# Kernel tuning notes

Hardware: AMD Instinct MI355X
Metric: run time of the kernel (lower is better)

## Reference

```python
import jax, jax.numpy as jnp
import numpy as np

D = 1024      # neural_dim
M = 8192      # memory_size (assumed fully used)
H = 16        # num_heads
B = 64        # batch
HD = D // H   # head dim


def setup_inputs() -> dict:
    key = jax.random.key(0)
    ks = jax.random.split(key, 24)
    s = 0.02
    inp = {
        "neural_input": jax.random.normal(ks[0], (B, D), jnp.float32),
        "memory_keys": jax.random.normal(ks[1], (M, D), jnp.float32),
        "memory_values": jax.random.normal(ks[2], (M, D), jnp.float32),
        # query/key/value projections (nn.Linear weights are [out, in])
        "Wq": jax.random.normal(ks[3], (D, D), jnp.float32) * s,
        "bq": jnp.zeros((D,), jnp.float32),
        "Wk": jax.random.normal(ks[4], (D, D), jnp.float32) * s,
        "bk": jnp.zeros((D,), jnp.float32),
        "Wv": jax.random.normal(ks[5], (D, D), jnp.float32) * s,
        "bv": jnp.zeros((D,), jnp.float32),
        # MultiheadAttention packed in-projection [3D, D] and out projection
        "in_proj_w": jax.random.normal(ks[6], (3 * D, D), jnp.float32) * s,
        "in_proj_b": jnp.zeros((3 * D,), jnp.float32),
        "out_w": jax.random.normal(ks[7], (D, D), jnp.float32) * s,
        "out_b": jnp.zeros((D,), jnp.float32),
        # memory_gate: Linear(2D->D), ReLU, Linear(D->D), Sigmoid
        "gW1": jax.random.normal(ks[8], (D, 2 * D), jnp.float32) * s,
        "gb1": jnp.zeros((D,), jnp.float32),
        "gW2": jax.random.normal(ks[9], (D, D), jnp.float32) * s,
        "gb2": jnp.zeros((D,), jnp.float32),
        # integration: Linear(2D->2D), ReLU, Linear(2D->D)
        "iW1": jax.random.normal(ks[10], (2 * D, 2 * D), jnp.float32) * s,
        "ib1": jnp.zeros((2 * D,), jnp.float32),
        "iW2": jax.random.normal(ks[11], (D, 2 * D), jnp.float32) * s,
        "ib2": jnp.zeros((D,), jnp.float32),
    }
    return inp


def reference(neural_input, memory_keys, memory_values,
              Wq, bq, Wk, bk, Wv, bv,
              in_proj_w, in_proj_b, out_w, out_b,
              gW1, gb1, gW2, gb2, iW1, ib1, iW2, ib2):
    x = neural_input  # [B, D]
    # pre-projections (memory_used assumed all True -> full tables)
    q = x @ Wq.T + bq                  # [B, D]
    k = memory_keys @ Wk.T + bk        # [M, D]
    v = memory_values @ Wv.T + bv      # [M, D]

    # MultiheadAttention (single query per batch element; K/V shared
    # across batch instead of the redundant expand in the original)
    Wiq, Wik, Wiv = in_proj_w[:D], in_proj_w[D:2 * D], in_proj_w[2 * D:]
    biq, bik, biv = in_proj_b[:D], in_proj_b[D:2 * D], in_proj_b[2 * D:]
    qh = (q @ Wiq.T + biq).reshape(B, H, HD)   # [B, H, hd]
    kh = (k @ Wik.T + bik).reshape(M, H, HD)   # [M, H, hd]
    vh = (v @ Wiv.T + biv).reshape(M, H, HD)   # [M, H, hd]

    scale = 1.0 / np.sqrt(HD).astype(np.float32)
    scores = jnp.einsum('bhd,mhd->bhm', qh, kh) * scale  # [B, H, M]
    attn = jax.nn.softmax(scores, axis=-1)
    ctx = jnp.einsum('bhm,mhd->bhd', attn, vh).reshape(B, D)
    memory_signal = ctx @ out_w.T + out_b      # [B, D]

    # gated fusion
    gate_in = jnp.concatenate([x, memory_signal], axis=-1)          # [B, 2D]
    gate = jax.nn.sigmoid(jax.nn.relu(gate_in @ gW1.T + gb1) @ gW2.T + gb2)
    gated_memory = gate * memory_signal
    combined = jnp.concatenate([x, gated_memory], axis=-1)          # [B, 2D]
    out = jax.nn.relu(combined @ iW1.T + ib1) @ iW2.T + ib2         # [B, D]
    return out
```

## Files before the change

### kernel.cpp

```cpp
#include <hip/hip_runtime.h>
#include <hip/hip_bf16.h>
#include <stdint.h>


typedef __bf16 bf16;
typedef __bf16 bf16x4 __attribute__((ext_vector_type(4)));
typedef __bf16 bf16x8 __attribute__((ext_vector_type(8)));
typedef float f32x4 __attribute__((ext_vector_type(4)));

#define D_ 1024
#define M_ 8192
#define B_ 64
#define H_ 16

static __device__ __forceinline__ void gload16(const void* g, void* l) {
  __builtin_amdgcn_global_load_lds(
      (const __attribute__((address_space(1))) void*)g,
      (__attribute__((address_space(3))) void*)l, 16, 0, 0);
}

static __device__ __forceinline__ f32x4 mfma16(bf16x8 a, bf16x8 b, f32x4 c) {
  return __builtin_amdgcn_mfma_f32_16x16x32_bf16(a, b, c, 0, 0, 0);
}

template <int U, int KLEN, typename OutT>
__device__ __forceinline__ void thin_gemm(
    const bf16* __restrict__ A, int lda,
    const bf16* __restrict__ Bm, int ldb,
    OutT* __restrict__ C, int ldc,
    const float* __restrict__ bias, float scale) {
  const int tid = threadIdx.x, lane = tid & 63, w = tid >> 6;
  const int rl = lane & 15, qq = lane >> 4;
  const bf16* pa = A + (int64_t)(w * 16 + rl) * lda + qq * 8;
  const bf16* pb[4];
  pb[0] = Bm + (int64_t)rl * ldb + qq * 8;
  pb[1] = pb[0] + (int64_t)16 * ldb;
  pb[2] = pb[0] + (int64_t)32 * ldb;
  pb[3] = pb[0] + (int64_t)48 * ldb;
  f32x4 acc[4] = {};
  bf16x8 av[2][U], bv[2][U][4];
#pragma unroll
  for (int u = 0; u < U; u++) {
    av[0][u] = *(const bf16x8*)(pa + u * 32);
#pragma unroll
    for (int j = 0; j < 4; j++)
      bv[0][u][j] = *(const bf16x8*)(pb[j] + u * 32);
  }
  constexpr int NI = KLEN / (32 * U);
#pragma unroll
  for (int it = 0; it < NI; it++) {
    const int cur = it & 1, nxt = cur ^ 1;
    if (it + 1 < NI) {
      int k = (it + 1) * 32 * U;
#pragma unroll
      for (int u = 0; u < U; u++) {
        av[nxt][u] = *(const bf16x8*)(pa + k + u * 32);
#pragma unroll
        for (int j = 0; j < 4; j++)
          bv[nxt][u][j] = *(const bf16x8*)(pb[j] + k + u * 32);
      }
    }
#pragma unroll
    for (int u = 0; u < U; u++)
#pragma unroll
      for (int j = 0; j < 4; j++)
        acc[j] = mfma16(av[cur][u], bv[cur][u][j], acc[j]);
  }
#pragma unroll
  for (int j = 0; j < 4; j++) {
    int gn = j * 16 + rl;
    float bb = bias ? bias[gn] : 0.0f;
#pragma unroll
    for (int r = 0; r < 4; r++) {
      int gm = w * 16 + qq * 4 + r;
      C[(int64_t)gm * ldc + gn] = (OutT)((acc[j][r] + bb) * scale);
    }
  }
}

struct CvtD { const float* src; bf16* dst; int end; };
struct PrepArgs {
  CvtD d[9];
  const float *Wq, *Wk, *Wv, *inw, *inb, *bq, *bk, *bv;
  bf16* WT;
  float* bc;
};

__global__ __launch_bounds__(256) void prep_kernel(PrepArgs a) {
  const int bx = blockIdx.x, tid = threadIdx.x;
  if (bx < 29760) {
    int g = bx * 256 + tid;
    CvtD dd = a.d[8];
    int begin = a.d[7].end;
#pragma unroll
    for (int t = 7; t >= 0; t--)
      if (g < a.d[t].end) { dd = a.d[t]; begin = t ? a.d[t - 1].end : 0; }
    int i = (g - begin) * 4;
    float4 v = *(const float4*)(dd.src + i);
    bf16x4 o = { (bf16)v.x, (bf16)v.y, (bf16)v.z, (bf16)v.w };
    *(bf16x4*)(dd.dst + i) = o;
  } else if (bx < 32832) {
    int t = bx - 29760;
    int z = t >> 10, rem = t & 1023;
    const float* src = z == 0 ? a.Wq : z == 1 ? a.Wk : a.Wv;
    bf16* out = a.WT + (int64_t)z * D_ * D_;
    __shared__ bf16 tile[32][33];
    int tx = tid & 31, ty = tid >> 5;
    int r0 = (rem >> 5) * 32, c0 = (rem & 31) * 32;
#pragma unroll
    for (int i = 0; i < 32; i += 8)
      tile[ty + i][tx] = (bf16)src[(int64_t)(r0 + ty + i) * D_ + c0 + tx];
    __syncthreads();
#pragma unroll
    for (int i = 0; i < 32; i += 8)
      out[(int64_t)(c0 + ty + i) * D_ + r0 + tx] = tile[tx][ty + i];
  } else {
    int t = bx - 32832;
    int w = tid >> 6, lane = tid & 63;
    int ng = t * 4 + w;
    int z = ng >> 10;
    const float* Wi = a.inw + (int64_t)ng * D_;
    const float* b = z == 0 ? a.bq : z == 1 ? a.bk : a.bv;
    float acc = 0.f;
#pragma unroll
    for (int l = 0; l < D_; l += 64) acc += Wi[l + lane] * b[l + lane];
#pragma unroll
    for (int m = 32; m; m >>= 1) acc += __shfl_xor(acc, m, 64);
    if (lane == 0) a.bc[ng] = acc + a.inb[ng];
  }
}

__global__ __launch_bounds__(256) void init_bias(
    const float* __restrict__ outb, const float* __restrict__ gb1,
    const float* __restrict__ gb2, const float* __restrict__ ib1,
    const float* __restrict__ ib2, float* __restrict__ msR,
    float* __restrict__ g1R, float* __restrict__ gateR,
    float* __restrict__ h1R, float* __restrict__ out) {
  int c = (blockIdx.x * 256 + threadIdx.x) * 4;
  int row = blockIdx.y;
  const float* b; float* dst; int n;
  if (c < 1024)      { b = outb; dst = msR   + row * 1024; n = c; }
  else if (c < 2048) { b = gb1;  dst = g1R   + row * 1024; n = c - 1024; }
  else if (c < 3072) { b = gb2;  dst = gateR + row * 1024; n = c - 2048; }
  else if (c < 5120) { b = ib1;  dst = h1R   + row * 2048; n = c - 3072; }
  else               { b = ib2;  dst = out   + row * 1024; n = c - 5120; }
  *(float4*)(dst + n) = *(const float4*)(b + n);
}

template <int MODE>
__global__ __launch_bounds__(256) void gemm_big(
    const bf16* __restrict__ A, int lda, int64_t sA,
    const bf16* __restrict__ Bm, int ldb, int64_t sB,
    bf16* __restrict__ C, int ldc, bf16* __restrict__ Ct,
    const float* __restrict__ bias, int64_t sbias, int K,
    const bf16* __restrict__ qA, const bf16* __restrict__ qB,
    bf16* __restrict__ qC, const float* __restrict__ qbias) {
  int m0, n0, z;
  if (MODE == 0) {
    z = blockIdx.z; m0 = blockIdx.y * 128; n0 = blockIdx.x * 128;
  } else {
    if ((int)blockIdx.x >= 1024) {
      int n0q = ((int)blockIdx.x - 1024) * 64;
      thin_gemm<2, 1024, bf16>(qA, D_, qB + (int64_t)n0q * D_, D_,
                               qC + n0q, D_, qbias + n0q, 0.125f);
      return;
    }
    int lin = blockIdx.x, xcd = lin & 7, slot = lin >> 3;
    z = slot >> 6;
    int r = slot & 63;
    m0 = (xcd * 8 + (r >> 3)) * 128;
    n0 = (r & 7) * 128;
  }
  A += (int64_t)z * sA; Bm += (int64_t)z * sB;
  if (bias) bias += (int64_t)z * sbias;
  __shared__ alignas(16) bf16 As[128 * 64];
  __shared__ alignas(16) bf16 Bs[128 * 64];
  const int tid = threadIdx.x, lane = tid & 63, w = tid >> 6;
  const int wm = (w & 1) * 64, wn = (w >> 1) * 64;
  const int rl = lane & 15, qq = lane >> 4;
  f32x4 acc[4][4] = {};

  const bf16 *gA[4], *gB[4];
  bf16 *lA[4], *lB[4];
#pragma unroll
  for (int it = 0; it < 4; it++) {
    int cc = it * 256 + w * 64 + lane;
    int r = cc >> 3, qp = cc & 7, q = qp ^ (r & 7);
    gA[it] = A + (int64_t)(m0 + r) * lda + q * 8;
    gB[it] = Bm + (int64_t)(n0 + r) * ldb + q * 8;
    lA[it] = As + (it * 256 + w * 64) * 8;
    lB[it] = Bs + (it * 256 + w * 64) * 8;
  }
  for (int k0 = 0; k0 < K; k0 += 64) {
    __syncthreads();
#pragma unroll
    for (int it = 0; it < 4; it++) {
      gload16(gA[it] + k0, lA[it]);
      gload16(gB[it] + k0, lB[it]);
    }
    __syncthreads();
#pragma unroll
    for (int kk = 0; kk < 2; kk++) {
      bf16x8 af[4], bb[4];
#pragma unroll
      for (int i = 0; i < 4; i++) {
        int ar = wm + i * 16 + rl;
        af[i] = *(const bf16x8*)(As + ar * 64 + (((kk * 4 + qq) ^ (ar & 7)) * 8));
      }
#pragma unroll
      for (int j = 0; j < 4; j++) {
        int br = wn + j * 16 + rl;
        bb[j] = *(const bf16x8*)(Bs + br * 64 + (((kk * 4 + qq) ^ (br & 7)) * 8));
      }
#pragma unroll
      for (int i = 0; i < 4; i++)
#pragma unroll
        for (int j = 0; j < 4; j++)
          acc[i][j] = mfma16(af[i], bb[j], acc[i][j]);
    }
  }
  if (MODE == 1 && z == 1) {
#pragma unroll
    for (int j = 0; j < 4; j++) {
      int gn = n0 + wn + j * 16 + rl;
      float bb = bias ? bias[gn] : 0.0f;
#pragma unroll
      for (int i = 0; i < 4; i++) {
        int gm0 = m0 + wm + i * 16 + qq * 4;
        f32x4 a = acc[i][j];
        bf16x4 o = { (bf16)(a[0] + bb), (bf16)(a[1] + bb),
                     (bf16)(a[2] + bb), (bf16)(a[3] + bb) };
        *(bf16x4*)(Ct + (int64_t)gn * M_ + gm0) = o;
      }
    }
  } else {
#pragma unroll
    for (int j = 0; j < 4; j++) {
      int gn = n0 + wn + j * 16 + rl;
      float bb = bias ? bias[gn] : 0.0f;
#pragma unroll
      for (int i = 0; i < 4; i++) {
        int gm0 = m0 + wm + i * 16 + qq * 4;
#pragma unroll
        for (int r = 0; r < 4; r++)
          C[(int64_t)(gm0 + r) * ldc + gn] = (bf16)(acc[i][j][r] + bb);
      }
    }
  }
}

__global__ __launch_bounds__(256) void flash_kernel(
    const bf16* __restrict__ qh, const bf16* __restrict__ kh,
    const bf16* __restrict__ vhT, float* __restrict__ opart,
    float* __restrict__ ml) {
  const int tid = threadIdx.x, lane = tid & 63, w = tid >> 6;
  const int rl = lane & 15, qq = lane >> 4;
  const int h = blockIdx.x >> 4, c = blockIdx.x & 15;
  __shared__ alignas(16) bf16 Plds[4 * 16 * 72];
  const bf16* qhp = qh + (int64_t)(w * 16 + rl) * D_ + h * 64 + qq * 8;
  bf16x8 aq0 = *(const bf16x8*)(qhp);
  bf16x8 aq1 = *(const bf16x8*)(qhp + 32);
  float m_st[4], l_st[4];
  f32x4 acc_o[4] = {};
#pragma unroll
  for (int r = 0; r < 4; r++) { m_st[r] = -3.0e38f; l_st[r] = 0.f; }
  bf16* pl = Plds + w * 1152;
  const bf16* khb = kh + (int64_t)(c * 512) * D_ + h * 64 + qq * 8;
  const bf16* vtb = vhT + (int64_t)(h * 64) * M_ + c * 512 + qq * 8;
  for (int nt = 0; nt < 8; nt++) {
    int mb = nt * 64;
    bf16x8 bk0[4], bk1[4];
#pragma unroll
    for (int j = 0; j < 4; j++) {
      const bf16* p = khb + (int64_t)(mb + j * 16 + rl) * D_;
      bk0[j] = *(const bf16x8*)(p);
      bk1[j] = *(const bf16x8*)(p + 32);
    }
    f32x4 s[4] = {};
#pragma unroll
    for (int j = 0; j < 4; j++) {
      s[j] = mfma16(aq0, bk0[j], s[j]);
      s[j] = mfma16(aq1, bk1[j], s[j]);
    }
    float rmax[4], alpha[4], rsum[4];
#pragma unroll
    for (int r = 0; r < 4; r++)
      rmax[r] = fmaxf(fmaxf(s[0][r], s[1][r]), fmaxf(s[2][r], s[3][r]));
#pragma unroll
    for (int msk = 1; msk <= 8; msk <<= 1)
#pragma unroll
      for (int r = 0; r < 4; r++)
        rmax[r] = fmaxf(rmax[r], __shfl_xor(rmax[r], msk, 64));
#pragma unroll
    for (int r = 0; r < 4; r++) {
      float mn = fmaxf(m_st[r], rmax[r]);
      alpha[r] = __expf(m_st[r] - mn);
      m_st[r] = mn;
      rsum[r] = 0.f;
    }
#pragma unroll
    for (int j = 0; j < 4; j++)
#pragma unroll
      for (int r = 0; r < 4; r++) {
        float p = __expf(s[j][r] - m_st[r]);
        rsum[r] += p;
        pl[(qq * 4 + r) * 72 + j * 16 + rl] = (bf16)p;
      }
#pragma unroll
    for (int msk = 1; msk <= 8; msk <<= 1)
#pragma unroll
      for (int r = 0; r < 4; r++) rsum[r] += __shfl_xor(rsum[r], msk, 64);
#pragma unroll
    for (int r = 0; r < 4; r++) l_st[r] = l_st[r] * alpha[r] + rsum[r];
#pragma unroll
    for (int j = 0; j < 4; j++)
#pragma unroll
      for (int r = 0; r < 4; r++) acc_o[j][r] *= alpha[r];
    bf16x8 pa0 = *(const bf16x8*)(pl + rl * 72 + qq * 8);
    bf16x8 pa1 = *(const bf16x8*)(pl + rl * 72 + 32 + qq * 8);
#pragma unroll
    for (int j = 0; j < 4; j++) {
      const bf16* q = vtb + (int64_t)(j * 16 + rl) * M_ + mb;
      bf16x8 v0 = *(const bf16x8*)(q);
      bf16x8 v1 = *(const bf16x8*)(q + 32);
      acc_o[j] = mfma16(pa0, v0, acc_o[j]);
      acc_o[j] = mfma16(pa1, v1, acc_o[j]);
    }
  }
  float* op = opart + (int64_t)(h * 16 + c) * 64 * 64;
#pragma unroll
  for (int j = 0; j < 4; j++)
#pragma unroll
    for (int r = 0; r < 4; r++)
      op[(w * 16 + qq * 4 + r) * 64 + j * 16 + rl] = acc_o[j][r];
  if (rl == 0) {
    float* mlp = ml + (int64_t)(h * 16 + c) * 128;
#pragma unroll
    for (int r = 0; r < 4; r++) {
      mlp[w * 16 + qq * 4 + r] = m_st[r];
      mlp[64 + w * 16 + qq * 4 + r] = l_st[r];
    }
  }
}

__global__ __launch_bounds__(256) void combine_kernel(
    const float* __restrict__ opart, const float* __restrict__ ml,
    bf16* __restrict__ ctx) {
  const int h = blockIdx.x >> 2, g = blockIdx.x & 3;
  const int d = threadIdx.x & 63;
#pragma unroll
  for (int it = 0; it < 4; it++) {
    int b = g * 16 + (threadIdx.x >> 6) + it * 4;
    float mstar = -3.0e38f;
    float mv_[16], lv_[16];
#pragma unroll
    for (int cc = 0; cc < 16; cc++) {
      mv_[cc] = ml[(int64_t)(h * 16 + cc) * 128 + b];
      lv_[cc] = ml[(int64_t)(h * 16 + cc) * 128 + 64 + b];
      mstar = fmaxf(mstar, mv_[cc]);
    }
    float lsum = 0.f, osum = 0.f;
#pragma unroll
    for (int cc = 0; cc < 16; cc++) {
      float f = __expf(mv_[cc] - mstar);
      lsum += lv_[cc] * f;
      osum += opart[((int64_t)(h * 16 + cc) * 64 + b) * 64 + d] * f;
    }
    ctx[(int64_t)b * D_ + h * 64 + d] = (bf16)(osum / lsum);
  }
}

struct Chunk { const void* p0; const void* p1; int ld; int kind; };
struct StageArgs { Chunk c[8]; };

__global__ __launch_bounds__(256) void tail_stage(
    StageArgs sa, const bf16* __restrict__ Bw, int ldb,
    float* __restrict__ Craw, int ldc) {
  const int n0 = blockIdx.x * 64, kc = blockIdx.y;
  const Chunk ch = sa.c[kc];
  const int tid = threadIdx.x, lane = tid & 63, w = tid >> 6;
  const int rl = lane & 15, qq = lane >> 4;
  const int m = w * 16 + rl;
  const bf16* pb[4];
#pragma unroll
  for (int j = 0; j < 4; j++)
    pb[j] = Bw + (int64_t)(n0 + j * 16 + rl) * ldb + kc * 256 + qq * 8;
  f32x4 acc[4] = {};
#pragma unroll
  for (int kk = 0; kk < 8; kk++) {
    bf16x8 af;
    if (ch.kind == 0) {
      af = *(const bf16x8*)((const bf16*)ch.p0 + (int64_t)m * ch.ld +
                            kk * 32 + qq * 8);
    } else {
      const float* p = (const float*)ch.p0 + (int64_t)m * ch.ld + kk * 32 + qq * 8;
      float4 u0 = *(const float4*)p;
      float4 u1 = *(const float4*)(p + 4);
      if (ch.kind == 2) {
        u0.x = fmaxf(u0.x, 0.f); u0.y = fmaxf(u0.y, 0.f);
        u0.z = fmaxf(u0.z, 0.f); u0.w = fmaxf(u0.w, 0.f);
        u1.x = fmaxf(u1.x, 0.f); u1.y = fmaxf(u1.y, 0.f);
        u1.z = fmaxf(u1.z, 0.f); u1.w = fmaxf(u1.w, 0.f);
      } else if (ch.kind == 3) {
        const float* pm = (const float*)ch.p1 + (int64_t)m * ch.ld + kk * 32 + qq * 8;
        float4 m0 = *(const float4*)pm;
        float4 m1 = *(const float4*)(pm + 4);
        u0.x = m0.x / (1.f + __expf(-u0.x)); u0.y = m0.y / (1.f + __expf(-u0.y));
        u0.z = m0.z / (1.f + __expf(-u0.z)); u0.w = m0.w / (1.f + __expf(-u0.w));
        u1.x = m1.x / (1.f + __expf(-u1.x)); u1.y = m1.y / (1.f + __expf(-u1.y));
        u1.z = m1.z / (1.f + __expf(-u1.z)); u1.w = m1.w / (1.f + __expf(-u1.w));
      }
      af = (bf16x8){ (bf16)u0.x, (bf16)u0.y, (bf16)u0.z, (bf16)u0.w,
                     (bf16)u1.x, (bf16)u1.y, (bf16)u1.z, (bf16)u1.w };
    }
    bf16x8 bf_[4];
#pragma unroll
    for (int j = 0; j < 4; j++) bf_[j] = *(const bf16x8*)(pb[j] + kk * 32);
#pragma unroll
    for (int j = 0; j < 4; j++) acc[j] = mfma16(af, bf_[j], acc[j]);
  }
#pragma unroll
  for (int j = 0; j < 4; j++) {
    int gn = n0 + j * 16 + rl;
#pragma unroll
    for (int r = 0; r < 4; r++) {
      int gm = w * 16 + qq * 4 + r;
      atomicAdd(&Craw[(int64_t)gm * ldc + gn], acc[j][r]);
    }
  }
}

extern "C" void kernel_launch(void* const* d_in, const int* in_sizes, int n_in,
                              void* d_out, int out_size, void* d_ws,
                              size_t ws_size, hipStream_t stream) {
  (void)in_sizes; (void)n_in; (void)out_size;
  const float* x    = (const float*)d_in[0];
  const float* mk   = (const float*)d_in[1];
  const float* mv   = (const float*)d_in[2];
  const float* Wq   = (const float*)d_in[3];
  const float* bq   = (const float*)d_in[4];
  const float* Wk   = (const float*)d_in[5];
  const float* bk   = (const float*)d_in[6];
  const float* Wv   = (const float*)d_in[7];
  const float* bv   = (const float*)d_in[8];
  const float* inw  = (const float*)d_in[9];
  const float* inb  = (const float*)d_in[10];
  const float* outw = (const float*)d_in[11];
  const float* outb = (const float*)d_in[12];
  const float* gW1  = (const float*)d_in[13];
  const float* gb1  = (const float*)d_in[14];
  const float* gW2  = (const float*)d_in[15];
  const float* gb2  = (const float*)d_in[16];
  const float* iW1  = (const float*)d_in[17];
  const float* ib1  = (const float*)d_in[18];
  const float* iW2  = (const float*)d_in[19];
  const float* ib2  = (const float*)d_in[20];

  char* ws = (char*)d_ws;
  size_t off = 0;
  auto alloc = [&](size_t bytes) {
    char* p = ws + off;
    off += (bytes + 255) & ~(size_t)255;
    return p;
  };
  bf16* mkmv  = (bf16*)alloc((size_t)2 * M_ * D_ * 2);
  bf16* inpj  = (bf16*)alloc((size_t)3 * D_ * D_ * 2);
  bf16* WT    = (bf16*)alloc((size_t)3 * D_ * D_ * 2);
  bf16* Wc    = (bf16*)alloc((size_t)3 * D_ * D_ * 2);
  float* bc   = (float*)alloc(3 * D_ * 4);
  bf16* xbf   = (bf16*)alloc((size_t)B_ * D_ * 2);
  bf16* qh    = (bf16*)alloc((size_t)B_ * D_ * 2);
  bf16* kh    = (bf16*)alloc((size_t)M_ * D_ * 2);
  bf16* vhT   = (bf16*)alloc((size_t)M_ * D_ * 2);
  float* opart= (float*)alloc((size_t)H_ * 16 * 64 * 64 * 4);
  float* ml   = (float*)alloc((size_t)H_ * 16 * 128 * 4);
  bf16* ctx   = (bf16*)alloc((size_t)B_ * D_ * 2);
  float* msR  = (float*)alloc((size_t)B_ * D_ * 4);
  float* g1R  = (float*)alloc((size_t)B_ * D_ * 4);
  float* gateR= (float*)alloc((size_t)B_ * D_ * 4);
  float* h1R  = (float*)alloc((size_t)B_ * 2 * D_ * 4);
  bf16* gW1b  = (bf16*)alloc((size_t)D_ * 2 * D_ * 2);
  bf16* gW2b  = (bf16*)alloc((size_t)D_ * D_ * 2);
  bf16* iW1b  = (bf16*)alloc((size_t)2 * D_ * 2 * D_ * 2);
  bf16* iW2b  = (bf16*)alloc((size_t)D_ * 2 * D_ * 2);
  bf16* outwb = (bf16*)alloc((size_t)D_ * D_ * 2);
  if (ws_size < off) return;

  PrepArgs pa;
  pa.d[0] = { mk,   mkmv,           2097152 };
  pa.d[1] = { mv,   mkmv + M_ * D_, 4194304 };
  pa.d[2] = { inw,  inpj,           4980736 };
  pa.d[3] = { gW1,  gW1b,           5505024 };
  pa.d[4] = { gW2,  gW2b,           5767168 };
  pa.d[5] = { iW1,  iW1b,           6815744 };
  pa.d[6] = { iW2,  iW2b,           7340032 };
  pa.d[7] = { outw, outwb,          7602176 };
  pa.d[8] = { x,    xbf,            7618560 };
  pa.Wq = Wq; pa.Wk = Wk; pa.Wv = Wv; pa.inw = inw; pa.inb = inb;
  pa.bq = bq; pa.bk = bk; pa.bv = bv; pa.WT = WT; pa.bc = bc;
  prep_kernel<<<dim3(33600), 256, 0, stream>>>(pa);

  init_bias<<<dim3(6, 64), 256, 0, stream>>>(outb, gb1, gb2, ib1, ib2,
                                             msR, g1R, gateR, h1R,
                                             (float*)d_out);

  gemm_big<0><<<dim3(8, 8, 3), 256, 0, stream>>>(
      inpj, D_, (int64_t)D_ * D_, WT, D_, (int64_t)D_ * D_,
      Wc, D_, nullptr, nullptr, 0, D_, nullptr, nullptr, nullptr, nullptr);

  gemm_big<1><<<dim3(1040), 256, 0, stream>>>(
      mkmv, D_, (int64_t)M_ * D_, Wc + (int64_t)D_ * D_, D_, (int64_t)D_ * D_,
      kh, D_, vhT, bc + D_, D_, D_,
      xbf, Wc, qh, bc);

  flash_kernel<<<dim3(256), 256, 0, stream>>>(qh, kh, vhT, opart, ml);
  combine_kernel<<<dim3(64), 256, 0, stream>>>(opart, ml, ctx);

  StageArgs s7;
  for (int kc = 0; kc < 4; kc++) s7.c[kc] = { ctx + kc * 256, nullptr, D_, 0 };
  tail_stage<<<dim3(16, 4), 256, 0, stream>>>(s7, outwb, D_, msR, D_);

  StageArgs s8;
  for (int kc = 0; kc < 4; kc++) s8.c[kc] = { xbf + kc * 256, nullptr, D_, 0 };
  for (int kc = 4; kc < 8; kc++) s8.c[kc] = { msR + (kc - 4) * 256, nullptr, D_, 1 };
  tail_stage<<<dim3(16, 8), 256, 0, stream>>>(s8, gW1b, 2 * D_, g1R, D_);

  StageArgs s9;
  for (int kc = 0; kc < 4; kc++) s9.c[kc] = { g1R + kc * 256, nullptr, D_, 2 };
  tail_stage<<<dim3(16, 4), 256, 0, stream>>>(s9, gW2b, D_, gateR, D_);

  StageArgs s10;
  for (int kc = 0; kc < 4; kc++) s10.c[kc] = { xbf + kc * 256, nullptr, D_, 0 };
  for (int kc = 4; kc < 8; kc++)
    s10.c[kc] = { gateR + (kc - 4) * 256, msR + (kc - 4) * 256, D_, 3 };
  tail_stage<<<dim3(32, 8), 256, 0, stream>>>(s10, iW1b, 2 * D_, h1R, 2 * D_);

  StageArgs s11;
  for (int kc = 0; kc < 8; kc++) s11.c[kc] = { h1R + kc * 256, nullptr, 2 * D_, 2 };
  tail_stage<<<dim3(16, 8), 256, 0, stream>>>(s11, iW2b, 2 * D_,
                                              (float*)d_out, D_);
}
```

Before: 381.4 us.

## Fuse attention and MLP tail into persistent kernel with grid barriers, shrink GEMM K-tile

Merges the flash attention, combine and five tail GEMM stages into one persistent 256-block kernel that steps through the stages using an atomic-counter grid barrier. It also folds the bias-init kernel into the prep kernel and halves the big GEMM K-tile from 64 to 32 with a new LDS swizzle. The aim is to cut kernel-launch overhead and give the big GEMM a smaller LDS footprint. In exchange it relies on all 256 blocks being resident at once for the spin barrier, and the smaller K-tile doubles the number of sync steps.

```diff
diff --git a/kernel.cpp b/kernel.cpp
--- a/kernel.cpp
+++ b/kernel.cpp
@@ -82,12 +82,15 @@
 struct PrepArgs {
   CvtD d[9];
   const float *Wq, *Wk, *Wv, *inw, *inb, *bq, *bk, *bv;
+  const float *outb, *gb1, *gb2, *ib1, *ib2;
   bf16* WT;
-  float* bc;
+  float *bc, *msR, *g1R, *gateR, *h1R, *out;
+  unsigned* bar;
 };
 
 __global__ __launch_bounds__(256) void prep_kernel(PrepArgs a) {
   const int bx = blockIdx.x, tid = threadIdx.x;
+  if (bx == 0 && tid == 0) *a.bar = 0u;
   if (bx < 29760) {
     int g = bx * 256 + tid;
     CvtD dd = a.d[8];
@@ -114,7 +117,7 @@
 #pragma unroll
     for (int i = 0; i < 32; i += 8)
       out[(int64_t)(c0 + ty + i) * D_ + r0 + tx] = tile[tx][ty + i];
-  } else {
+  } else if (bx < 33600) {
     int t = bx - 32832;
     int w = tid >> 6, lane = tid & 63;
     int ng = t * 4 + w;
@@ -127,31 +130,28 @@
 #pragma unroll
     for (int m = 32; m; m >>= 1) acc += __shfl_xor(acc, m, 64);
     if (lane == 0) a.bc[ng] = acc + a.inb[ng];
-  }
-}
-
-__global__ __launch_bounds__(256) void init_bias(
-    const float* __restrict__ outb, const float* __restrict__ gb1,
-    const float* __restrict__ gb2, const float* __restrict__ ib1,
-    const float* __restrict__ ib2, float* __restrict__ msR,
-    float* __restrict__ g1R, float* __restrict__ gateR,
-    float* __restrict__ h1R, float* __restrict__ out) {
-  int c = (blockIdx.x * 256 + threadIdx.x) * 4;
-  int row = blockIdx.y;
-  const float* b; float* dst; int n;
-  if (c < 1024)      { b = outb; dst = msR   + row * 1024; n = c; }
-  else if (c < 2048) { b = gb1;  dst = g1R   + row * 1024; n = c - 1024; }
-  else if (c < 3072) { b = gb2;  dst = gateR + row * 1024; n = c - 2048; }
-  else if (c < 5120) { b = ib1;  dst = h1R   + row * 2048; n = c - 3072; }
-  else               { b = ib2;  dst = out   + row * 1024; n = c - 5120; }
-  *(float4*)(dst + n) = *(const float4*)(b + n);
+  } else {
+    int t = bx - 33600;
+    int seg = t >> 6, row = t & 63;
+    int n = tid * 4;
+    const float* b;
+    float* dst;
+    int bn = n;
+    if (seg == 0)      { dst = a.msR   + row * 1024;        b = a.outb; }
+    else if (seg == 1) { dst = a.g1R   + row * 1024;        b = a.gb1;  }
+    else if (seg == 2) { dst = a.gateR + row * 1024;        b = a.gb2;  }
+    else if (seg == 3) { dst = a.h1R   + row * 2048;        b = a.ib1;  }
+    else if (seg == 4) { dst = a.h1R   + row * 2048 + 1024; b = a.ib1; bn = 1024 + n; }
+    else               { dst = a.out   + row * 1024;        b = a.ib2;  }
+    *(float4*)(dst + n) = *(const float4*)(b + bn);
+  }
 }
 
 template <int MODE>
 __global__ __launch_bounds__(256) void gemm_big(
     const bf16* __restrict__ A, int lda, int64_t sA,
     const bf16* __restrict__ Bm, int ldb, int64_t sB,
-    bf16* __restrict__ C, int ldc, bf16* __restrict__ Ct,
+    bf16* __restrict__ C, int ldc, int64_t sC, bf16* __restrict__ Ct,
     const float* __restrict__ bias, int64_t sbias, int K,
     const bf16* __restrict__ qA, const bf16* __restrict__ qB,
     bf16* __restrict__ qC, const float* __restrict__ qbias) {
@@ -173,236 +173,110 @@
   }
   A += (int64_t)z * sA; Bm += (int64_t)z * sB;
   if (bias) bias += (int64_t)z * sbias;
-  __shared__ alignas(16) bf16 As[128 * 64];
-  __shared__ alignas(16) bf16 Bs[128 * 64];
+  __shared__ alignas(16) bf16 As[128 * 32];
+  __shared__ alignas(16) bf16 Bs[128 * 32];
   const int tid = threadIdx.x, lane = tid & 63, w = tid >> 6;
   const int wm = (w & 1) * 64, wn = (w >> 1) * 64;
   const int rl = lane & 15, qq = lane >> 4;
   f32x4 acc[4][4] = {};
 
-  const bf16 *gA[4], *gB[4];
-  bf16 *lA[4], *lB[4];
-#pragma unroll
-  for (int it = 0; it < 4; it++) {
-    int cc = it * 256 + w * 64 + lane;
-    int r = cc >> 3, qp = cc & 7, q = qp ^ (r & 7);
-    gA[it] = A + (int64_t)(m0 + r) * lda + q * 8;
-    gB[it] = Bm + (int64_t)(n0 + r) * ldb + q * 8;
-    lA[it] = As + (it * 256 + w * 64) * 8;
-    lB[it] = Bs + (it * 256 + w * 64) * 8;
-  }
-  for (int k0 = 0; k0 < K; k0 += 64) {
+  int c0 = w * 64 + lane, c1 = (4 + w) * 64 + lane;
+  int ra0 = c0 >> 2, qa0 = (c0 & 3) ^ ((ra0 >> 1) & 3);
+  int ra1 = c1 >> 2, qa1 = (c1 & 3) ^ ((ra1 >> 1) & 3);
+  const bf16* gA0 = A + (int64_t)(m0 + ra0) * lda + qa0 * 8;
+  const bf16* gA1 = A + (int64_t)(m0 + ra1) * lda + qa1 * 8;
+  const bf16* gB0 = Bm + (int64_t)(n0 + ra0) * ldb + qa0 * 8;
+  const bf16* gB1 = Bm + (int64_t)(n0 + ra1) * ldb + qa1 * 8;
+  bf16* lA0 = As + w * 512;
+  bf16* lA1 = As + (4 + w) * 512;
+  bf16* lB0 = Bs + w * 512;
+  bf16* lB1 = Bs + (4 + w) * 512;
+
+  for (int k0 = 0; k0 < K; k0 += 32) {
     __syncthreads();
-#pragma unroll
-    for (int it = 0; it < 4; it++) {
-      gload16(gA[it] + k0, lA[it]);
-      gload16(gB[it] + k0, lB[it]);
-    }
+    gload16(gA0 + k0, lA0);
+    gload16(gA1 + k0, lA1);
+    gload16(gB0 + k0, lB0);
+    gload16(gB1 + k0, lB1);
     __syncthreads();
-#pragma unroll
-    for (int kk = 0; kk < 2; kk++) {
-      bf16x8 af[4], bb[4];
-#pragma unroll
-      for (int i = 0; i < 4; i++) {
-        int ar = wm + i * 16 + rl;
-        af[i] = *(const bf16x8*)(As + ar * 64 + (((kk * 4 + qq) ^ (ar & 7)) * 8));
-      }
-#pragma unroll
-      for (int j = 0; j < 4; j++) {
-        int br = wn + j * 16 + rl;
-        bb[j] = *(const bf16x8*)(Bs + br * 64 + (((kk * 4 + qq) ^ (br & 7)) * 8));
-      }
-#pragma unroll
-      for (int i = 0; i < 4; i++)
-#pragma unroll
-        for (int j = 0; j < 4; j++)
-          acc[i][j] = mfma16(af[i], bb[j], acc[i][j]);
-    }
+    bf16x8 af[4], bb[4];
+#pragma unroll
+    for (int i = 0; i < 4; i++) {
+      int r = wm + i * 16 + rl;
+      af[i] = *(const bf16x8*)(As + r * 32 + (qq ^ ((r >> 1) & 3)) * 8);
+    }
+#pragma unroll
+    for (int j = 0; j < 4; j++) {
+      int r = wn + j * 16 + rl;
+      bb[j] = *(const bf16x8*)(Bs + r * 32 + (qq ^ ((r >> 1) & 3)) * 8);
+    }
+#pragma unroll
+    for (int i = 0; i < 4; i++)
+#pragma unroll
+      for (int j = 0; j < 4; j++)
+        acc[i][j] = mfma16(af[i], bb[j], acc[i][j]);
   }
   if (MODE == 1 && z == 1) {
 #pragma unroll
     for (int j = 0; j < 4; j++) {
       int gn = n0 + wn + j * 16 + rl;
-      float bb = bias ? bias[gn] : 0.0f;
+      float bb2 = bias ? bias[gn] : 0.0f;
 #pragma unroll
       for (int i = 0; i < 4; i++) {
         int gm0 = m0 + wm + i * 16 + qq * 4;
         f32x4 a = acc[i][j];
-        bf16x4 o = { (bf16)(a[0] + bb), (bf16)(a[1] + bb),
-                     (bf16)(a[2] + bb), (bf16)(a[3] + bb) };
+        bf16x4 o = { (bf16)(a[0] + bb2), (bf16)(a[1] + bb2),
+                     (bf16)(a[2] + bb2), (bf16)(a[3] + bb2) };
         *(bf16x4*)(Ct + (int64_t)gn * M_ + gm0) = o;
       }
     }
   } else {
+    C += (int64_t)z * sC;
 #pragma unroll
     for (int j = 0; j < 4; j++) {
       int gn = n0 + wn + j * 16 + rl;
-      float bb = bias ? bias[gn] : 0.0f;
+      float bb2 = bias ? bias[gn] : 0.0f;
 #pragma unroll
       for (int i = 0; i < 4; i++) {
         int gm0 = m0 + wm + i * 16 + qq * 4;
 #pragma unroll
         for (int r = 0; r < 4; r++)
-          C[(int64_t)(gm0 + r) * ldc + gn] = (bf16)(acc[i][j][r] + bb);
-      }
-    }
-  }
-}
-
-__global__ __launch_bounds__(256) void flash_kernel(
-    const bf16* __restrict__ qh, const bf16* __restrict__ kh,
-    const bf16* __restrict__ vhT, float* __restrict__ opart,
-    float* __restrict__ ml) {
-  const int tid = threadIdx.x, lane = tid & 63, w = tid >> 6;
-  const int rl = lane & 15, qq = lane >> 4;
-  const int h = blockIdx.x >> 4, c = blockIdx.x & 15;
-  __shared__ alignas(16) bf16 Plds[4 * 16 * 72];
-  const bf16* qhp = qh + (int64_t)(w * 16 + rl) * D_ + h * 64 + qq * 8;
-  bf16x8 aq0 = *(const bf16x8*)(qhp);
-  bf16x8 aq1 = *(const bf16x8*)(qhp + 32);
-  float m_st[4], l_st[4];
-  f32x4 acc_o[4] = {};
-#pragma unroll
-  for (int r = 0; r < 4; r++) { m_st[r] = -3.0e38f; l_st[r] = 0.f; }
-  bf16* pl = Plds + w * 1152;
-  const bf16* khb = kh + (int64_t)(c * 512) * D_ + h * 64 + qq * 8;
-  const bf16* vtb = vhT + (int64_t)(h * 64) * M_ + c * 512 + qq * 8;
-  for (int nt = 0; nt < 8; nt++) {
-    int mb = nt * 64;
-    bf16x8 bk0[4], bk1[4];
-#pragma unroll
-    for (int j = 0; j < 4; j++) {
-      const bf16* p = khb + (int64_t)(mb + j * 16 + rl) * D_;
-      bk0[j] = *(const bf16x8*)(p);
-      bk1[j] = *(const bf16x8*)(p + 32);
-    }
-    f32x4 s[4] = {};
-#pragma unroll
-    for (int j = 0; j < 4; j++) {
-      s[j] = mfma16(aq0, bk0[j], s[j]);
-      s[j] = mfma16(aq1, bk1[j], s[j]);
-    }
-    float rmax[4], alpha[4], rsum[4];
-#pragma unroll
-    for (int r = 0; r < 4; r++)
-      rmax[r] = fmaxf(fmaxf(s[0][r], s[1][r]), fmaxf(s[2][r], s[3][r]));
-#pragma unroll
-    for (int msk = 1; msk <= 8; msk <<= 1)
-#pragma unroll
-      for (int r = 0; r < 4; r++)
-        rmax[r] = fmaxf(rmax[r], __shfl_xor(rmax[r], msk, 64));
-#pragma unroll
-    for (int r = 0; r < 4; r++) {
-      float mn = fmaxf(m_st[r], rmax[r]);
-      alpha[r] = __expf(m_st[r] - mn);
-      m_st[r] = mn;
-      rsum[r] = 0.f;
-    }
-#pragma unroll
-    for (int j = 0; j < 4; j++)
-#pragma unroll
-      for (int r = 0; r < 4; r++) {
-        float p = __expf(s[j][r] - m_st[r]);
-        rsum[r] += p;
-        pl[(qq * 4 + r) * 72 + j * 16 + rl] = (bf16)p;
-      }
-#pragma unroll
-    for (int msk = 1; msk <= 8; msk <<= 1)
-#pragma unroll
-      for (int r = 0; r < 4; r++) rsum[r] += __shfl_xor(rsum[r], msk, 64);
-#pragma unroll
-    for (int r = 0; r < 4; r++) l_st[r] = l_st[r] * alpha[r] + rsum[r];
-#pragma unroll
-    for (int j = 0; j < 4; j++)
-#pragma unroll
-      for (int r = 0; r < 4; r++) acc_o[j][r] *= alpha[r];
-    bf16x8 pa0 = *(const bf16x8*)(pl + rl * 72 + qq * 8);
-    bf16x8 pa1 = *(const bf16x8*)(pl + rl * 72 + 32 + qq * 8);
-#pragma unroll
-    for (int j = 0; j < 4; j++) {
-      const bf16* q = vtb + (int64_t)(j * 16 + rl) * M_ + mb;
-      bf16x8 v0 = *(const bf16x8*)(q);
-      bf16x8 v1 = *(const bf16x8*)(q + 32);
-      acc_o[j] = mfma16(pa0, v0, acc_o[j]);
-      acc_o[j] = mfma16(pa1, v1, acc_o[j]);
-    }
-  }
-  float* op = opart + (int64_t)(h * 16 + c) * 64 * 64;
-#pragma unroll
-  for (int j = 0; j < 4; j++)
-#pragma unroll
-    for (int r = 0; r < 4; r++)
-      op[(w * 16 + qq * 4 + r) * 64 + j * 16 + rl] = acc_o[j][r];
-  if (rl == 0) {
-    float* mlp = ml + (int64_t)(h * 16 + c) * 128;
-#pragma unroll
-    for (int r = 0; r < 4; r++) {
-      mlp[w * 16 + qq * 4 + r] = m_st[r];
-      mlp[64 + w * 16 + qq * 4 + r] = l_st[r];
-    }
-  }
-}
-
-__global__ __launch_bounds__(256) void combine_kernel(
-    const float* __restrict__ opart, const float* __restrict__ ml,
-    bf16* __restrict__ ctx) {
-  const int h = blockIdx.x >> 2, g = blockIdx.x & 3;
-  const int d = threadIdx.x & 63;
-#pragma unroll
-  for (int it = 0; it < 4; it++) {
-    int b = g * 16 + (threadIdx.x >> 6) + it * 4;
-    float mstar = -3.0e38f;
-    float mv_[16], lv_[16];
-#pragma unroll
-    for (int cc = 0; cc < 16; cc++) {
-      mv_[cc] = ml[(int64_t)(h * 16 + cc) * 128 + b];
-      lv_[cc] = ml[(int64_t)(h * 16 + cc) * 128 + 64 + b];
-      mstar = fmaxf(mstar, mv_[cc]);
-    }
-    float lsum = 0.f, osum = 0.f;
-#pragma unroll
-    for (int cc = 0; cc < 16; cc++) {
-      float f = __expf(mv_[cc] - mstar);
-      lsum += lv_[cc] * f;
-      osum += opart[((int64_t)(h * 16 + cc) * 64 + b) * 64 + d] * f;
-    }
-    ctx[(int64_t)b * D_ + h * 64 + d] = (bf16)(osum / lsum);
-  }
-}
-
-struct Chunk { const void* p0; const void* p1; int ld; int kind; };
-struct StageArgs { Chunk c[8]; };
-
-__global__ __launch_bounds__(256) void tail_stage(
-    StageArgs sa, const bf16* __restrict__ Bw, int ldb,
+          C[(int64_t)(gm0 + r) * ldc + gn] = (bf16)(acc[i][j][r] + bb2);
+      }
+    }
+  }
+}
+
+template <int KIND, int NKK>
+static __device__ __forceinline__ void stage_mm(
+    const void* __restrict__ p0, const void* __restrict__ p1, int lda,
+    const bf16* __restrict__ Bw, int ldb, int bk0, int n0,
     float* __restrict__ Craw, int ldc) {
-  const int n0 = blockIdx.x * 64, kc = blockIdx.y;
-  const Chunk ch = sa.c[kc];
   const int tid = threadIdx.x, lane = tid & 63, w = tid >> 6;
   const int rl = lane & 15, qq = lane >> 4;
   const int m = w * 16 + rl;
   const bf16* pb[4];
 #pragma unroll
   for (int j = 0; j < 4; j++)
-    pb[j] = Bw + (int64_t)(n0 + j * 16 + rl) * ldb + kc * 256 + qq * 8;
+    pb[j] = Bw + (int64_t)(n0 + j * 16 + rl) * ldb + bk0 + qq * 8;
   f32x4 acc[4] = {};
 #pragma unroll
-  for (int kk = 0; kk < 8; kk++) {
+  for (int kk = 0; kk < NKK; kk++) {
     bf16x8 af;
-    if (ch.kind == 0) {
-      af = *(const bf16x8*)((const bf16*)ch.p0 + (int64_t)m * ch.ld +
-                            kk * 32 + qq * 8);
+    if constexpr (KIND == 0) {
+      af = *(const bf16x8*)((const bf16*)p0 + (int64_t)m * lda + kk * 32 + qq * 8);
     } else {
-      const float* p = (const float*)ch.p0 + (int64_t)m * ch.ld + kk * 32 + qq * 8;
+      const float* p = (const float*)p0 + (int64_t)m * lda + kk * 32 + qq * 8;
       float4 u0 = *(const float4*)p;
       float4 u1 = *(const float4*)(p + 4);
-      if (ch.kind == 2) {
+      if constexpr (KIND == 2) {
         u0.x = fmaxf(u0.x, 0.f); u0.y = fmaxf(u0.y, 0.f);
         u0.z = fmaxf(u0.z, 0.f); u0.w = fmaxf(u0.w, 0.f);
         u1.x = fmaxf(u1.x, 0.f); u1.y = fmaxf(u1.y, 0.f);
         u1.z = fmaxf(u1.z, 0.f); u1.w = fmaxf(u1.w, 0.f);
-      } else if (ch.kind == 3) {
-        const float* pm = (const float*)ch.p1 + (int64_t)m * ch.ld + kk * 32 + qq * 8;
+      }
+      if constexpr (KIND == 3) {
+        const float* pm = (const float*)p1 + (int64_t)m * lda + kk * 32 + qq * 8;
         float4 m0 = *(const float4*)pm;
         float4 m1 = *(const float4*)(pm + 4);
         u0.x = m0.x / (1.f + __expf(-u0.x)); u0.y = m0.y / (1.f + __expf(-u0.y));
@@ -427,6 +301,192 @@
       int gm = w * 16 + qq * 4 + r;
       atomicAdd(&Craw[(int64_t)gm * ldc + gn], acc[j][r]);
     }
+  }
+}
+
+struct TailArgs {
+  const bf16 *qh, *kh, *vhT, *xbf;
+  float *opart, *ml;
+  bf16* ctx;
+  const bf16 *outwb, *gW1b, *gW2b, *iW1b, *iW2b;
+  float *msR, *g1R, *gateR, *h1R, *out;
+  unsigned* bar;
+};
+
+static __device__ __forceinline__ void grid_sync(unsigned* bar, unsigned target) {
+  __syncthreads();
+  if (threadIdx.x == 0) {
+    __threadfence();
+    atomicAdd(bar, 1u);
+    while (__hip_atomic_load(bar, __ATOMIC_RELAXED, __HIP_MEMORY_SCOPE_AGENT) <
+           target)
+      __builtin_amdgcn_s_sleep(2);
+    __threadfence();
+  }
+  __syncthreads();
+}
+
+__global__ __launch_bounds__(256, 1) void tail_mega(TailArgs ta) {
+  const int bx = blockIdx.x;
+  const int tid = threadIdx.x, lane = tid & 63, w = tid >> 6;
+  const int rl = lane & 15, qq = lane >> 4;
+  __shared__ alignas(16) bf16 Plds[4 * 16 * 72];
+
+  {
+    const int h = bx >> 4, c = bx & 15;
+    const bf16* qhp = ta.qh + (int64_t)(w * 16 + rl) * D_ + h * 64 + qq * 8;
+    bf16x8 aq0 = *(const bf16x8*)(qhp);
+    bf16x8 aq1 = *(const bf16x8*)(qhp + 32);
+    float m_st[4], l_st[4];
+    f32x4 acc_o[4] = {};
+#pragma unroll
+    for (int r = 0; r < 4; r++) { m_st[r] = -3.0e38f; l_st[r] = 0.f; }
+    bf16* pl = Plds + w * 1152;
+    const bf16* khb = ta.kh + (int64_t)(c * 512) * D_ + h * 64 + qq * 8;
+    const bf16* vtb = ta.vhT + (int64_t)(h * 64) * M_ + c * 512 + qq * 8;
+    for (int nt = 0; nt < 8; nt++) {
+      int mb = nt * 64;
+      bf16x8 bk0[4], bk1[4];
+#pragma unroll
+      for (int j = 0; j < 4; j++) {
+        const bf16* p = khb + (int64_t)(mb + j * 16 + rl) * D_;
+        bk0[j] = *(const bf16x8*)(p);
+        bk1[j] = *(const bf16x8*)(p + 32);
+      }
+      f32x4 s[4] = {};
+#pragma unroll
+      for (int j = 0; j < 4; j++) {
+        s[j] = mfma16(aq0, bk0[j], s[j]);
+        s[j] = mfma16(aq1, bk1[j], s[j]);
+      }
+      float rmax[4], alpha[4], rsum[4];
+#pragma unroll
+      for (int r = 0; r < 4; r++)
+        rmax[r] = fmaxf(fmaxf(s[0][r], s[1][r]), fmaxf(s[2][r], s[3][r]));
+#pragma unroll
+      for (int msk = 1; msk <= 8; msk <<= 1)
+#pragma unroll
+        for (int r = 0; r < 4; r++)
+          rmax[r] = fmaxf(rmax[r], __shfl_xor(rmax[r], msk, 64));
+#pragma unroll
+      for (int r = 0; r < 4; r++) {
+        float mn = fmaxf(m_st[r], rmax[r]);
+        alpha[r] = __expf(m_st[r] - mn);
+        m_st[r] = mn;
+        rsum[r] = 0.f;
+      }
+#pragma unroll
+      for (int j = 0; j < 4; j++)
+#pragma unroll
+        for (int r = 0; r < 4; r++) {
+          float p = __expf(s[j][r] - m_st[r]);
+          rsum[r] += p;
+          pl[(qq * 4 + r) * 72 + j * 16 + rl] = (bf16)p;
+        }
+#pragma unroll
+      for (int msk = 1; msk <= 8; msk <<= 1)
+#pragma unroll
+        for (int r = 0; r < 4; r++) rsum[r] += __shfl_xor(rsum[r], msk, 64);
+#pragma unroll
+      for (int r = 0; r < 4; r++) l_st[r] = l_st[r] * alpha[r] + rsum[r];
+#pragma unroll
+      for (int j = 0; j < 4; j++)
+#pragma unroll
+        for (int r = 0; r < 4; r++) acc_o[j][r] *= alpha[r];
+      bf16x8 pa0 = *(const bf16x8*)(pl + rl * 72 + qq * 8);
+      bf16x8 pa1 = *(const bf16x8*)(pl + rl * 72 + 32 + qq * 8);
+#pragma unroll
+      for (int j = 0; j < 4; j++) {
+        const bf16* q = vtb + (int64_t)(j * 16 + rl) * M_ + mb;
+        bf16x8 v0 = *(const bf16x8*)(q);
+        bf16x8 v1 = *(const bf16x8*)(q + 32);
+        acc_o[j] = mfma16(pa0, v0, acc_o[j]);
+        acc_o[j] = mfma16(pa1, v1, acc_o[j]);
+      }
+    }
+    float* op = ta.opart + (int64_t)(h * 16 + c) * 64 * 64;
+#pragma unroll
+    for (int j = 0; j < 4; j++)
+#pragma unroll
+      for (int r = 0; r < 4; r++)
+        op[(w * 16 + qq * 4 + r) * 64 + j * 16 + rl] = acc_o[j][r];
+    if (rl == 0) {
+      float* mlp = ta.ml + (int64_t)(h * 16 + c) * 128;
+#pragma unroll
+      for (int r = 0; r < 4; r++) {
+        mlp[w * 16 + qq * 4 + r] = m_st[r];
+        mlp[64 + w * 16 + qq * 4 + r] = l_st[r];
+      }
+    }
+  }
+  grid_sync(ta.bar, 256);
+
+  if (bx < 64) {
+    const int h = bx >> 2, g = bx & 3;
+    const int d = tid & 63;
+#pragma unroll
+    for (int it = 0; it < 4; it++) {
+      int b = g * 16 + (tid >> 6) + it * 4;
+      float mstar = -3.0e38f;
+      float mv_[16], lv_[16];
+#pragma unroll
+      for (int cc = 0; cc < 16; cc++) {
+        mv_[cc] = ta.ml[(int64_t)(h * 16 + cc) * 128 + b];
+        lv_[cc] = ta.ml[(int64_t)(h * 16 + cc) * 128 + 64 + b];
+        mstar = fmaxf(mstar, mv_[cc]);
+      }
+      float lsum = 0.f, osum = 0.f;
+#pragma unroll
+      for (int cc = 0; cc < 16; cc++) {
+        float f = __expf(mv_[cc] - mstar);
+        lsum += lv_[cc] * f;
+        osum += ta.opart[((int64_t)(h * 16 + cc) * 64 + b) * 64 + d] * f;
+      }
+      ta.ctx[(int64_t)b * D_ + h * 64 + d] = (bf16)(osum / lsum);
+    }
+  }
+  grid_sync(ta.bar, 512);
+
+  {
+    int n0 = (bx >> 4) * 64, kc = bx & 15;
+    stage_mm<0, 2>(ta.ctx + kc * 64, nullptr, D_, ta.outwb, D_, kc * 64, n0,
+                   ta.msR, D_);
+  }
+  grid_sync(ta.bar, 768);
+
+  {
+    int n0 = (bx >> 4) * 64, kc = bx & 15;
+    if (kc < 8)
+      stage_mm<0, 4>(ta.xbf + kc * 128, nullptr, D_, ta.gW1b, 2048, kc * 128,
+                     n0, ta.g1R, D_);
+    else
+      stage_mm<1, 4>(ta.msR + (kc - 8) * 128, nullptr, D_, ta.gW1b, 2048,
+                     1024 + (kc - 8) * 128, n0, ta.g1R, D_);
+  }
+  grid_sync(ta.bar, 1024);
+
+  {
+    int n0 = (bx >> 4) * 64, kc = bx & 15;
+    stage_mm<2, 2>(ta.g1R + kc * 64, nullptr, D_, ta.gW2b, D_, kc * 64, n0,
+                   ta.gateR, D_);
+  }
+  grid_sync(ta.bar, 1280);
+
+  {
+    int n0 = (bx >> 3) * 64, kc = bx & 7;
+    if (kc < 4)
+      stage_mm<0, 8>(ta.xbf + kc * 256, nullptr, D_, ta.iW1b, 2048, kc * 256,
+                     n0, ta.h1R, 2048);
+    else
+      stage_mm<3, 8>(ta.gateR + (kc - 4) * 256, ta.msR + (kc - 4) * 256, D_,
+                     ta.iW1b, 2048, 1024 + (kc - 4) * 256, n0, ta.h1R, 2048);
+  }
+  grid_sync(ta.bar, 1536);
+
+  {
+    int n0 = (bx >> 4) * 64, kc = bx & 15;
+    stage_mm<2, 4>(ta.h1R + kc * 128, nullptr, 2048, ta.iW2b, 2048, kc * 128,
+                   n0, ta.out, D_);
   }
 }
 
@@ -484,6 +544,7 @@
   bf16* iW1b  = (bf16*)alloc((size_t)2 * D_ * 2 * D_ * 2);
   bf16* iW2b  = (bf16*)alloc((size_t)D_ * 2 * D_ * 2);
   bf16* outwb = (bf16*)alloc((size_t)D_ * D_ * 2);
+  unsigned* bar = (unsigned*)alloc(256);
   if (ws_size < off) return;
 
   PrepArgs pa;
@@ -497,46 +558,28 @@
   pa.d[7] = { outw, outwb,          7602176 };
   pa.d[8] = { x,    xbf,            7618560 };
   pa.Wq = Wq; pa.Wk = Wk; pa.Wv = Wv; pa.inw = inw; pa.inb = inb;
-  pa.bq = bq; pa.bk = bk; pa.bv = bv; pa.WT = WT; pa.bc = bc;
-  prep_kernel<<<dim3(33600), 256, 0, stream>>>(pa);
-
-  init_bias<<<dim3(6, 64), 256, 0, stream>>>(outb, gb1, gb2, ib1, ib2,
-                                             msR, g1R, gateR, h1R,
-                                             (float*)d_out);
+  pa.bq = bq; pa.bk = bk; pa.bv = bv;
+  pa.outb = outb; pa.gb1 = gb1; pa.gb2 = gb2; pa.ib1 = ib1; pa.ib2 = ib2;
+  pa.WT = WT; pa.bc = bc; pa.msR = msR; pa.g1R = g1R; pa.gateR = gateR;
+  pa.h1R = h1R; pa.out = (float*)d_out; pa.bar = bar;
+  prep_kernel<<<dim3(33984), 256, 0, stream>>>(pa);
 
   gemm_big<0><<<dim3(8, 8, 3), 256, 0, stream>>>(
       inpj, D_, (int64_t)D_ * D_, WT, D_, (int64_t)D_ * D_,
-      Wc, D_, nullptr, nullptr, 0, D_, nullptr, nullptr, nullptr, nullptr);
+      Wc, D_, (int64_t)D_ * D_, nullptr, nullptr, 0, D_,
+      nullptr, nullptr, nullptr, nullptr);
 
   gemm_big<1><<<dim3(1040), 256, 0, stream>>>(
       mkmv, D_, (int64_t)M_ * D_, Wc + (int64_t)D_ * D_, D_, (int64_t)D_ * D_,
-      kh, D_, vhT, bc + D_, D_, D_,
+      kh, D_, 0, vhT, bc + D_, D_, D_,
       xbf, Wc, qh, bc);
 
-  flash_kernel<<<dim3(256), 256, 0, stream>>>(qh, kh, vhT, opart, ml);
-  combine_kernel<<<dim3(64), 256, 0, stream>>>(opart, ml, ctx);
-
-  StageArgs s7;
-  for (int kc = 0; kc < 4; kc++) s7.c[kc] = { ctx + kc * 256, nullptr, D_, 0 };
-  tail_stage<<<dim3(16, 4), 256, 0, stream>>>(s7, outwb, D_, msR, D_);
-
-  StageArgs s8;
-  for (int kc = 0; kc < 4; kc++) s8.c[kc] = { xbf + kc * 256, nullptr, D_, 0 };
-  for (int kc = 4; kc < 8; kc++) s8.c[kc] = { msR + (kc - 4) * 256, nullptr, D_, 1 };
-  tail_stage<<<dim3(16, 8), 256, 0, stream>>>(s8, gW1b, 2 * D_, g1R, D_);
-
-  StageArgs s9;
-  for (int kc = 0; kc < 4; kc++) s9.c[kc] = { g1R + kc * 256, nullptr, D_, 2 };
-  tail_stage<<<dim3(16, 4), 256, 0, stream>>>(s9, gW2b, D_, gateR, D_);
-
-  StageArgs s10;
-  for (int kc = 0; kc < 4; kc++) s10.c[kc] = { xbf + kc * 256, nullptr, D_, 0 };
-  for (int kc = 4; kc < 8; kc++)
-    s10.c[kc] = { gateR + (kc - 4) * 256, msR + (kc - 4) * 256, D_, 3 };
-  tail_stage<<<dim3(32, 8), 256, 0, stream>>>(s10, iW1b, 2 * D_, h1R, 2 * D_);
-
-  StageArgs s11;
-  for (int kc = 0; kc < 8; kc++) s11.c[kc] = { h1R + kc * 256, nullptr, 2 * D_, 2 };
-  tail_stage<<<dim3(16, 8), 256, 0, stream>>>(s11, iW2b, 2 * D_,
-                                              (float*)d_out, D_);
-}
+  TailArgs ta;
+  ta.qh = qh; ta.kh = kh; ta.vhT = vhT; ta.xbf = xbf;
+  ta.opart = opart; ta.ml = ml; ta.ctx = ctx;
+  ta.outwb = outwb; ta.gW1b = gW1b; ta.gW2b = gW2b;
+  ta.iW1b = iW1b; ta.iW2b = iW2b;
+  ta.msR = msR; ta.g1R = g1R; ta.gateR = gateR; ta.h1R = h1R;
+  ta.out = (float*)d_out; ta.bar = bar;
+  tail_mega<<<dim3(256), 256, 0, stream>>>(ta);
+}
```

Result: slower. 465.2 us (+22.0%).
